# Kernel optimization log

Measured on AMD Instinct MI355X. Metric: run time of the kernel, lower is better.

Reference implementation:

```python
import jax, jax.numpy as jnp
import numpy as np

T = 1024      # tokens
H = 2048      # hidden_size
I = 1408      # moe_intermediate_size
E = 16        # n_routed_experts
K = 6         # num_experts_per_tok
SI = I * 2    # shared experts intermediate (n_shared_experts=2)


def setup_inputs() -> dict:
    key = jax.random.key(0)
    ks = jax.random.split(key, 8)
    s = 0.02
    return {
        "x": jax.random.normal(ks[0], (T, H), jnp.float32),
        "gate_w": jax.random.normal(ks[1], (E, H), jnp.float32) * s,
        "w_gate": jax.random.normal(ks[2], (E, I, H), jnp.float32) * s,
        "w_up": jax.random.normal(ks[3], (E, I, H), jnp.float32) * s,
        "w_down": jax.random.normal(ks[4], (E, H, I), jnp.float32) * s,
        "sw_gate": jax.random.normal(ks[5], (SI, H), jnp.float32) * s,
        "sw_up": jax.random.normal(ks[6], (SI, H), jnp.float32) * s,
        "sw_down": jax.random.normal(ks[7], (H, SI), jnp.float32) * s,
    }


def reference(x, gate_w, w_gate, w_up, w_down, sw_gate, sw_up, sw_down):
    t = x.shape[0]
    # ---- router: softmax over experts, top-k, renormalize (norm_topk_prob) ----
    logits = x @ gate_w.T                                   # [T, E]
    probs = jax.nn.softmax(logits.astype(jnp.float32), axis=-1)
    topw, topi = jax.lax.top_k(probs, K)                    # [T, K]
    topw = topw / jnp.sum(topw, axis=-1, keepdims=True)
    # per-token per-expert combine weight (0 for unselected experts)
    comb = jnp.zeros((t, E), probs.dtype).at[
        jnp.arange(t)[:, None], topi
    ].add(topw)                                             # [T, E]

    # ---- routed experts: SwiGLU MLP per expert, weighted combine ----
    g = jnp.einsum('th,eih->tei', x, w_gate)                # [T, E, I]
    u = jnp.einsum('th,eih->tei', x, w_up)                  # [T, E, I]
    h = jax.nn.silu(g) * u                                  # [T, E, I]
    routed = jnp.einsum('te,tei,ehi->th', comb, h, w_down)  # [T, H]

    # ---- shared experts (always-on SwiGLU MLP) ----
    shared = (jax.nn.silu(x @ sw_gate.T) * (x @ sw_up.T)) @ sw_down.T  # [T, H]

    return routed + shared
```

## Files before the change

### kernel.cpp

```cpp
#include <hip/hip_runtime.h>
#include <stdint.h>

#define T_TOK 1024
#define H_DIM 2048
#define I_DIM 1408
#define E_NUM 16
#define K_TOP 6
#define PADCAP 8192
#define NE_ALL 18

typedef __attribute__((ext_vector_type(8))) short short8;
typedef __attribute__((ext_vector_type(8))) unsigned short ushort8;
typedef __attribute__((ext_vector_type(4))) float f32x4;

__device__ __forceinline__ unsigned short f2b(float f) {
    unsigned u = __float_as_uint(f);
    u += 0x7fffu + ((u >> 16) & 1u);
    return (unsigned short)(u >> 16);
}
__device__ __forceinline__ float b2f(unsigned short s) {
    return __uint_as_float((unsigned)s << 16);
}

__device__ __forceinline__ unsigned cvt_pk2(float a, float b) {
    unsigned r;
    asm("v_cvt_pk_bf16_f32 %0, %1, %2" : "=v"(r) : "v"(a), "v"(b));
    return r;
}

typedef __attribute__((address_space(1))) const unsigned int as1_uint;
typedef __attribute__((address_space(3))) unsigned int as3_uint;
__device__ __forceinline__ void gload16(const void* g, void* l) {
    __builtin_amdgcn_global_load_lds((as1_uint*)g, (as3_uint*)l, 16, 0, 0);
}

__device__ __forceinline__ int xcd_swizzle(int bid, int nwg) {
    const int q = nwg >> 3, r = nwg & 7;
    const int xcd = bid & 7, k = bid >> 3;
    const int base = (xcd < r) ? xcd * (q + 1) : r * (q + 1) + (xcd - r) * q;
    return base + k;
}

__global__ __launch_bounds__(256) void router_kernel(
    const float* __restrict__ x, const float* __restrict__ gw,
    float* __restrict__ topw, int* __restrict__ eidx, int* __restrict__ slotarr,
    int* __restrict__ counts)
{
    const int t = blockIdx.x, tid = threadIdx.x;
    const int lane = tid & 63, wave = tid >> 6;
    float part[E_NUM];
#pragma unroll
    for (int e = 0; e < E_NUM; ++e) part[e] = 0.f;
    const float* xr = x + (size_t)t * H_DIM;
    for (int i = tid; i < H_DIM; i += 256) {
        float xv = xr[i];
#pragma unroll
        for (int e = 0; e < E_NUM; ++e) part[e] += xv * gw[e * H_DIM + i];
    }
    __shared__ float red[4][E_NUM];
#pragma unroll
    for (int e = 0; e < E_NUM; ++e) {
        float v = part[e];
        for (int off = 32; off; off >>= 1) v += __shfl_down(v, off);
        if (lane == 0) red[wave][e] = v;
    }
    __syncthreads();
    if (tid == 0) {
        float logits[E_NUM];
#pragma unroll
        for (int e = 0; e < E_NUM; ++e)
            logits[e] = red[0][e] + red[1][e] + red[2][e] + red[3][e];
        int sel[K_TOP]; float selv[K_TOP];
        unsigned used = 0;
        for (int k = 0; k < K_TOP; ++k) {
            int best = 0; float bv = -1e30f;
            for (int e = 0; e < E_NUM; ++e)
                if (!((used >> e) & 1u) && logits[e] > bv) { bv = logits[e]; best = e; }
            used |= 1u << best; sel[k] = best; selv[k] = bv;
        }
        float mx = selv[0], s = 0.f, w[K_TOP];
        for (int k = 0; k < K_TOP; ++k) { w[k] = expf(selv[k] - mx); s += w[k]; }
        float inv = 1.f / s;
        for (int k = 0; k < K_TOP; ++k) {
            int slot = atomicAdd(&counts[sel[k]], 1);
            topw[t * K_TOP + k] = w[k] * inv;
            eidx[t * K_TOP + k] = sel[k];
            slotarr[t * K_TOP + k] = slot;
        }
    }
}

__global__ void zero_counts_kernel(int* counts) {
    if (threadIdx.x < E_NUM) counts[threadIdx.x] = 0;
}

__global__ void prefix_kernel(const int* __restrict__ counts, int* __restrict__ offs) {
    if (threadIdx.x == 0) {
        int o = 0;
        for (int e = 0; e < E_NUM; ++e) { offs[e] = o; o += (counts[e] + 127) & ~127; }
        offs[E_NUM] = o;
    }
}

__global__ __launch_bounds__(256) void gather_cvt_kernel(
    const float* __restrict__ x, const int* __restrict__ eidx,
    const int* __restrict__ slotarr, const int* __restrict__ offs,
    ushort* __restrict__ Xall)
{
    const int b = blockIdx.x;
    int t; size_t row;
    if (b < T_TOK * K_TOP) {
        t = b / K_TOP;
        row = (size_t)offs[eidx[b]] + (size_t)slotarr[b];
    } else {
        t = b - T_TOK * K_TOP;
        row = (size_t)offs[E_NUM] + (size_t)t;
    }
    const float* src = x + (size_t)t * H_DIM;
    ushort* dst = Xall + row * H_DIM;
    const int i = threadIdx.x * 8;
    float4 f0 = *(const float4*)(src + i);
    float4 f1 = *(const float4*)(src + i + 4);
    ushort8 v;
    v[0] = f2b(f0.x); v[1] = f2b(f0.y); v[2] = f2b(f0.z); v[3] = f2b(f0.w);
    v[4] = f2b(f1.x); v[5] = f2b(f1.y); v[6] = f2b(f1.z); v[7] = f2b(f1.w);
    *(ushort8*)(dst + i) = v;
}

template<int DOWN>
__global__ __launch_bounds__(256, 2) void moe_gemm_kernel(
    const ushort* __restrict__ Abase,
    const float* __restrict__ Wr1, const float* __restrict__ Wr2,
    const float* __restrict__ Ws1, const float* __restrict__ Ws2,
    ushort* __restrict__ C1, ushort* __restrict__ C2,
    const int* __restrict__ counts, const int* __restrict__ offs,
    int nNT, int K, int ldc)
{
    __shared__ short Alds[2][128 * 64];
    __shared__ short Blds[2][128 * 64];

    const int work = xcd_swizzle(blockIdx.x, gridDim.x);
    const int slab = NE_ALL * 8;
    int nt = work / slab;
    const int rem = work - nt * slab;
    const int e = rem >> 3;
    const int mt = rem & 7;

    const int S = offs[E_NUM];
    const int M = (e < E_NUM) ? counts[e] : 1024;
    const int row0 = mt << 7;
    if (row0 >= M) return;
    const int crowbase = (e < E_NUM) ? offs[e] : S + ((e - E_NUM) << 10);
    const int arowbase = DOWN ? crowbase : ((e < E_NUM) ? offs[e] : S);

    const float* B; ushort* C; int ldb;
    if (DOWN) {
        ldb = (e < E_NUM) ? I_DIM : 2 * I_DIM;
        B = (e < E_NUM) ? Wr1 + (size_t)e * H_DIM * I_DIM
                        : Ws1 + (size_t)(e - E_NUM) * I_DIM;
        C = C1;
    } else {
        ldb = H_DIM;
        const float* Bg = (e < E_NUM) ? Wr1 + (size_t)e * I_DIM * H_DIM
                                      : Ws1 + (size_t)(e - E_NUM) * I_DIM * H_DIM;
        const float* Bu = (e < E_NUM) ? Wr2 + (size_t)e * I_DIM * H_DIM
                                      : Ws2 + (size_t)(e - E_NUM) * I_DIM * H_DIM;
        if (nt < nNT) { B = Bg; C = C1; }
        else          { B = Bu; C = C2; nt -= nNT; }
    }
    const int n0 = nt << 7;

    const int tid = threadIdx.x;
    const int lane = tid & 63;
    const int wave = tid >> 6;
    const int wm = wave & 1, wn = wave >> 1;
    const int l15 = lane & 15, lhi = lane >> 4;

    const char* __restrict__ Ab = (const char*)(Abase + (size_t)(arowbase + row0) * K);

    int aOff[4];
#pragma unroll
    for (int i = 0; i < 4; ++i) {
        const int chunk = wave * 4 + i;
        const int off = chunk * 1024 + lane * 16;
        const int r = off >> 7, s = (off >> 4) & 7;
        aOff[i] = r * K * 2 + ((s ^ (r & 7)) << 4);
    }

    const int r0 = (wave << 5) + (lane >> 3);
    const int sl = lane & 7;
    const float* Bg0 = B + (size_t)(n0 + r0) * ldb + (sl << 3);
    const int bLds0 = (r0 << 6) + ((sl ^ (r0 & 7)) << 3);

    f32x4 acc[4][4];
#pragma unroll
    for (int m = 0; m < 4; ++m)
#pragma unroll
        for (int n = 0; n < 4; ++n) acc[m][n] = (f32x4){0.f, 0.f, 0.f, 0.f};

    float4 breg[4][2];
    auto issueB = [&](int k0) {
#pragma unroll
        for (int j = 0; j < 4; ++j) {
            const float* src = Bg0 + (size_t)(j << 3) * ldb + k0;
            breg[j][0] = *(const float4*)src;
            breg[j][1] = *(const float4*)(src + 4);
        }
    };
    auto issueA = [&](int pb, int k0) {
#pragma unroll
        for (int i = 0; i < 4; ++i)
            gload16(Ab + (size_t)aOff[i] + (size_t)k0 * 2,
                    (char*)Alds[pb] + (wave * 4 + i) * 1024);
    };
    auto writeB = [&](int pb) {
        short* bl = Blds[pb];
#pragma unroll
        for (int j = 0; j < 4; ++j) {
            union { short8 s; unsigned u[4]; } w;
            w.u[0] = cvt_pk2(breg[j][0].x, breg[j][0].y);
            w.u[1] = cvt_pk2(breg[j][0].z, breg[j][0].w);
            w.u[2] = cvt_pk2(breg[j][1].x, breg[j][1].y);
            w.u[3] = cvt_pk2(breg[j][1].z, breg[j][1].w);
            *(short8*)&bl[bLds0 + (j << 9)] = w.s;
        }
    };

    const int nK = K >> 6;
    issueB(0);
    issueA(0, 0);
    writeB(0);
    __syncthreads();

    int p = 0;
    for (int kt = 0; kt < nK; ++kt) {
        const bool more = (kt + 1 < nK);
        if (more) {
            issueB((kt + 1) << 6);
            issueA(p ^ 1, (kt + 1) << 6);
        }
#pragma unroll
        for (int kk = 0; kk < 2; ++kk) {
            const int kb = (kk << 2) + lhi;
            short8 af[4], bfr[4];
#pragma unroll
            for (int m = 0; m < 4; ++m) {
                const int rA = (wm << 6) + (m << 4) + l15;
                af[m] = *(const short8*)&Alds[p][(rA << 6) + ((kb ^ (rA & 7)) << 3)];
            }
#pragma unroll
            for (int n = 0; n < 4; ++n) {
                const int rB = (wn << 6) + (n << 4) + l15;
                bfr[n] = *(const short8*)&Blds[p][(rB << 6) + ((kb ^ (rB & 7)) << 3)];
            }
#pragma unroll
            for (int m = 0; m < 4; ++m)
#pragma unroll
                for (int n = 0; n < 4; ++n)
                    acc[m][n] = __builtin_amdgcn_mfma_f32_16x16x32_bf16(
                        af[m], bfr[n], acc[m][n], 0, 0, 0);
        }
        if (more) writeB(p ^ 1);
        __syncthreads();
        p ^= 1;
    }

    const size_t cbase_col = (size_t)n0 + (wn << 6) + l15;
#pragma unroll
    for (int m = 0; m < 4; ++m) {
        const int rloc = (wm << 6) + (m << 4) + (lhi << 2);
#pragma unroll
        for (int j = 0; j < 4; ++j) {
            const int crow = row0 + rloc + j;
            if (crow >= M) continue;
            const size_t co = (size_t)(crowbase + crow) * ldc + cbase_col;
#pragma unroll
            for (int n = 0; n < 4; ++n) C[co + (n << 4)] = f2b(acc[m][n][j]);
        }
    }
}

__global__ __launch_bounds__(256) void silu_kernel(
    ushort* __restrict__ G, const ushort* __restrict__ U,
    const int* __restrict__ eidx, const int* __restrict__ slotarr,
    const int* __restrict__ offs)
{
    const int b = blockIdx.x;
    size_t row;
    if (b < T_TOK * K_TOP) {
        row = (size_t)offs[eidx[b]] + (size_t)slotarr[b];
    } else {
        row = (size_t)offs[E_NUM] + (size_t)(b - T_TOK * K_TOP);
    }
    ushort* g = G + row * I_DIM;
    const ushort* u = U + row * I_DIM;
    for (int i = threadIdx.x * 8; i < I_DIM; i += 2048) {
        ushort8 gv = *(const ushort8*)(g + i);
        ushort8 uv = *(const ushort8*)(u + i);
        ushort8 hv;
#pragma unroll
        for (int j = 0; j < 8; ++j) {
            float gf = b2f(gv[j]);
            float uf = b2f(uv[j]);
            float sf = gf / (1.f + expf(-gf));
            hv[j] = f2b(sf * uf);
        }
        *(ushort8*)(g + i) = hv;
    }
}

__global__ __launch_bounds__(256) void combine_kernel(
    float* __restrict__ out, const ushort* __restrict__ Y,
    const float* __restrict__ topw, const int* __restrict__ eidx,
    const int* __restrict__ slotarr, const int* __restrict__ offs)
{
    const int t = blockIdx.x;
    const int i = threadIdx.x * 8;
    const int S = offs[E_NUM];
    float acc[8];
    {
        ushort8 v0 = *(const ushort8*)(Y + ((size_t)S + t) * H_DIM + i);
        ushort8 v1 = *(const ushort8*)(Y + ((size_t)S + 1024 + t) * H_DIM + i);
#pragma unroll
        for (int j = 0; j < 8; ++j) acc[j] = b2f(v0[j]) + b2f(v1[j]);
    }
#pragma unroll
    for (int k = 0; k < K_TOP; ++k) {
        const float w = topw[t * K_TOP + k];
        const size_t row = (size_t)offs[eidx[t * K_TOP + k]] + (size_t)slotarr[t * K_TOP + k];
        ushort8 v = *(const ushort8*)(Y + row * H_DIM + i);
#pragma unroll
        for (int j = 0; j < 8; ++j) acc[j] += w * b2f(v[j]);
    }
    float* o = out + (size_t)t * H_DIM;
    float4 o0, o1;
    o0.x = acc[0]; o0.y = acc[1]; o0.z = acc[2]; o0.w = acc[3];
    o1.x = acc[4]; o1.y = acc[5]; o1.z = acc[6]; o1.w = acc[7];
    *(float4*)(o + i) = o0;
    *(float4*)(o + i + 4) = o1;
}

extern "C" void kernel_launch(void* const* d_in, const int* in_sizes, int n_in,
                              void* d_out, int out_size, void* d_ws, size_t ws_size,
                              hipStream_t stream) {
    const float* x       = (const float*)d_in[0];
    const float* gate_w  = (const float*)d_in[1];
    const float* w_gate  = (const float*)d_in[2];
    const float* w_up    = (const float*)d_in[3];
    const float* w_down  = (const float*)d_in[4];
    const float* sw_gate = (const float*)d_in[5];
    const float* sw_up   = (const float*)d_in[6];
    const float* sw_down = (const float*)d_in[7];
    float* out = (float*)d_out;

    char* p = (char*)d_ws;
    auto take = [&](size_t b) { char* r = p; p += (b + 255) & ~(size_t)255; return r; };
    int*    counts = (int*)take(32 * 4);
    int*    offs   = (int*)take(32 * 4);
    float*  topw   = (float*)take((size_t)T_TOK * K_TOP * 4);
    int*    eidx   = (int*)take((size_t)T_TOK * K_TOP * 4);
    int*    slot   = (int*)take((size_t)T_TOK * K_TOP * 4);
    ushort* Xall   = (ushort*)take((size_t)(PADCAP + 1024) * H_DIM * 2);
    ushort* G      = (ushort*)take((size_t)(PADCAP + 2048) * I_DIM * 2);
    ushort* U      = (ushort*)take((size_t)(PADCAP + 2048) * I_DIM * 2);
    ushort* Y      = (ushort*)take((size_t)(PADCAP + 2048) * H_DIM * 2);

    zero_counts_kernel<<<1, 64, 0, stream>>>(counts);
    router_kernel<<<T_TOK, 256, 0, stream>>>(x, gate_w, topw, eidx, slot, counts);
    prefix_kernel<<<1, 64, 0, stream>>>(counts, offs);
    gather_cvt_kernel<<<T_TOK * K_TOP + T_TOK, 256, 0, stream>>>(x, eidx, slot, offs, Xall);

    moe_gemm_kernel<0><<<22 * NE_ALL * 8, 256, 0, stream>>>(
        Xall, w_gate, w_up, sw_gate, sw_up, G, U, counts, offs, 11, H_DIM, I_DIM);
    silu_kernel<<<T_TOK * K_TOP + 2048, 256, 0, stream>>>(G, U, eidx, slot, offs);
    moe_gemm_kernel<1><<<16 * NE_ALL * 8, 256, 0, stream>>>(
        G, w_down, nullptr, sw_down, nullptr, Y, nullptr, counts, offs, 16, I_DIM, H_DIM);

    combine_kernel<<<T_TOK, 256, 0, stream>>>(out, Y, topw, eidx, slot, offs);
}
```

Baseline: 557.7 us.

## Enlarge MoE GEMM tiles to 256x128 with 512 threads and register-pipelined B

The MoE GEMM kernel now launches 512 threads per block and covers 256 token rows per tile instead of 128. This halves the number of M-tiles per expert, so each fp32 weight tile is fetched and converted to bf16 half as often. B now uses a single LDS buffer and is double-buffered in registers, while A stays double-buffered in LDS. Synchronisation uses explicit s_waitcnt and s_barrier, and the loop is unrolled by two. The trade-offs are more LDS and registers per block, which may lower occupancy, and more wasted rows on experts with few tokens.

```diff
diff --git a/kernel.cpp b/kernel.cpp
--- a/kernel.cpp
+++ b/kernel.cpp
@@ -33,6 +33,9 @@
 __device__ __forceinline__ void gload16(const void* g, void* l) {
     __builtin_amdgcn_global_load_lds((as1_uint*)g, (as3_uint*)l, 16, 0, 0);
 }
+
+#define WAIT_A_LGKM() asm volatile("s_waitcnt vmcnt(4) lgkmcnt(0)" ::: "memory")
+#define BAR() __builtin_amdgcn_s_barrier()
 
 __device__ __forceinline__ int xcd_swizzle(int bid, int nwg) {
     const int q = nwg >> 3, r = nwg & 7;
@@ -128,7 +131,7 @@
 }
 
 template<int DOWN>
-__global__ __launch_bounds__(256, 2) void moe_gemm_kernel(
+__global__ __launch_bounds__(512, 2) void moe_gemm_kernel(
     const ushort* __restrict__ Abase,
     const float* __restrict__ Wr1, const float* __restrict__ Wr2,
     const float* __restrict__ Ws1, const float* __restrict__ Ws2,
@@ -136,19 +139,19 @@
     const int* __restrict__ counts, const int* __restrict__ offs,
     int nNT, int K, int ldc)
 {
-    __shared__ short Alds[2][128 * 64];
-    __shared__ short Blds[2][128 * 64];
+    __shared__ short Alds[2][256 * 64];
+    __shared__ short Blds[128 * 64];
 
     const int work = xcd_swizzle(blockIdx.x, gridDim.x);
-    const int slab = NE_ALL * 8;
+    const int slab = NE_ALL * 4;
     int nt = work / slab;
     const int rem = work - nt * slab;
-    const int e = rem >> 3;
-    const int mt = rem & 7;
+    const int e = rem >> 2;
+    const int mt = rem & 3;
 
     const int S = offs[E_NUM];
     const int M = (e < E_NUM) ? counts[e] : 1024;
-    const int row0 = mt << 7;
+    const int row0 = mt << 8;
     if (row0 >= M) return;
     const int crowbase = (e < E_NUM) ? offs[e] : S + ((e - E_NUM) << 10);
     const int arowbase = DOWN ? crowbase : ((e < E_NUM) ? offs[e] : S);
@@ -173,7 +176,7 @@
     const int tid = threadIdx.x;
     const int lane = tid & 63;
     const int wave = tid >> 6;
-    const int wm = wave & 1, wn = wave >> 1;
+    const int wm = wave >> 1, wn = wave & 1;
     const int l15 = lane & 15, lhi = lane >> 4;
 
     const char* __restrict__ Ab = (const char*)(Abase + (size_t)(arowbase + row0) * K);
@@ -187,10 +190,15 @@
         aOff[i] = r * K * 2 + ((s ^ (r & 7)) << 4);
     }
 
-    const int r0 = (wave << 5) + (lane >> 3);
-    const int sl = lane & 7;
-    const float* Bg0 = B + (size_t)(n0 + r0) * ldb + (sl << 3);
-    const int bLds0 = (r0 << 6) + ((sl ^ (r0 & 7)) << 3);
+    const float* Bcell[2];
+    int bld[2];
+#pragma unroll
+    for (int c = 0; c < 2; ++c) {
+        const int cell = tid + (c << 9);
+        const int row = cell >> 3, sl = cell & 7;
+        Bcell[c] = B + (size_t)(n0 + row) * ldb + (sl << 3);
+        bld[c] = (row << 6) + ((sl ^ (row & 7)) << 3);
+    }
 
     f32x4 acc[4][4];
 #pragma unroll
@@ -198,47 +206,34 @@
 #pragma unroll
         for (int n = 0; n < 4; ++n) acc[m][n] = (f32x4){0.f, 0.f, 0.f, 0.f};
 
-    float4 breg[4][2];
-    auto issueB = [&](int k0) {
-#pragma unroll
-        for (int j = 0; j < 4; ++j) {
-            const float* src = Bg0 + (size_t)(j << 3) * ldb + k0;
-            breg[j][0] = *(const float4*)src;
-            breg[j][1] = *(const float4*)(src + 4);
-        }
-    };
-    auto issueA = [&](int pb, int k0) {
+    float4 brA[2][2], brB[2][2];
+
+    auto issueA = [&](int kt, int pb) {
 #pragma unroll
         for (int i = 0; i < 4; ++i)
-            gload16(Ab + (size_t)aOff[i] + (size_t)k0 * 2,
+            gload16(Ab + (size_t)aOff[i] + (size_t)(kt << 6) * 2,
                     (char*)Alds[pb] + (wave * 4 + i) * 1024);
     };
-    auto writeB = [&](int pb) {
-        short* bl = Blds[pb];
-#pragma unroll
-        for (int j = 0; j < 4; ++j) {
+    auto issueB = [&](int kt, float4 (&br)[2][2]) {
+#pragma unroll
+        for (int c = 0; c < 2; ++c) {
+            const float* src = Bcell[c] + (kt << 6);
+            br[c][0] = *(const float4*)src;
+            br[c][1] = *(const float4*)(src + 4);
+        }
+    };
+    auto writeB = [&](float4 (&br)[2][2]) {
+#pragma unroll
+        for (int c = 0; c < 2; ++c) {
             union { short8 s; unsigned u[4]; } w;
-            w.u[0] = cvt_pk2(breg[j][0].x, breg[j][0].y);
-            w.u[1] = cvt_pk2(breg[j][0].z, breg[j][0].w);
-            w.u[2] = cvt_pk2(breg[j][1].x, breg[j][1].y);
-            w.u[3] = cvt_pk2(breg[j][1].z, breg[j][1].w);
-            *(short8*)&bl[bLds0 + (j << 9)] = w.s;
+            w.u[0] = cvt_pk2(br[c][0].x, br[c][0].y);
+            w.u[1] = cvt_pk2(br[c][0].z, br[c][0].w);
+            w.u[2] = cvt_pk2(br[c][1].x, br[c][1].y);
+            w.u[3] = cvt_pk2(br[c][1].z, br[c][1].w);
+            *(short8*)&Blds[bld[c]] = w.s;
         }
     };
-
-    const int nK = K >> 6;
-    issueB(0);
-    issueA(0, 0);
-    writeB(0);
-    __syncthreads();
-
-    int p = 0;
-    for (int kt = 0; kt < nK; ++kt) {
-        const bool more = (kt + 1 < nK);
-        if (more) {
-            issueB((kt + 1) << 6);
-            issueA(p ^ 1, (kt + 1) << 6);
-        }
+    auto compute = [&](int p) {
 #pragma unroll
         for (int kk = 0; kk < 2; ++kk) {
             const int kb = (kk << 2) + lhi;
@@ -251,7 +246,7 @@
 #pragma unroll
             for (int n = 0; n < 4; ++n) {
                 const int rB = (wn << 6) + (n << 4) + l15;
-                bfr[n] = *(const short8*)&Blds[p][(rB << 6) + ((kb ^ (rB & 7)) << 3)];
+                bfr[n] = *(const short8*)&Blds[(rB << 6) + ((kb ^ (rB & 7)) << 3)];
             }
 #pragma unroll
             for (int m = 0; m < 4; ++m)
@@ -260,9 +255,32 @@
                     acc[m][n] = __builtin_amdgcn_mfma_f32_16x16x32_bf16(
                         af[m], bfr[n], acc[m][n], 0, 0, 0);
         }
-        if (more) writeB(p ^ 1);
-        __syncthreads();
-        p ^= 1;
+    };
+
+    const int nK = K >> 6;
+    issueB(0, brA);
+    issueA(0, 0);
+    writeB(brA);
+    issueB(nK > 1 ? 1 : 0, brB);
+    WAIT_A_LGKM();
+    BAR();
+
+    for (int tt = 0; tt < nK; tt += 2) {
+        issueA(min(tt + 1, nK - 1), 1);
+        issueB(min(tt + 2, nK - 1), brA);
+        compute(0);
+        BAR();
+        writeB(brB);
+        WAIT_A_LGKM();
+        BAR();
+
+        issueA(min(tt + 2, nK - 1), 0);
+        issueB(min(tt + 3, nK - 1), brB);
+        compute(1);
+        BAR();
+        writeB(brA);
+        WAIT_A_LGKM();
+        BAR();
     }
 
     const size_t cbase_col = (size_t)n0 + (wn << 6) + l15;
@@ -370,10 +388,10 @@
     prefix_kernel<<<1, 64, 0, stream>>>(counts, offs);
     gather_cvt_kernel<<<T_TOK * K_TOP + T_TOK, 256, 0, stream>>>(x, eidx, slot, offs, Xall);
 
-    moe_gemm_kernel<0><<<22 * NE_ALL * 8, 256, 0, stream>>>(
+    moe_gemm_kernel<0><<<22 * NE_ALL * 4, 512, 0, stream>>>(
         Xall, w_gate, w_up, sw_gate, sw_up, G, U, counts, offs, 11, H_DIM, I_DIM);
     silu_kernel<<<T_TOK * K_TOP + 2048, 256, 0, stream>>>(G, U, eidx, slot, offs);
-    moe_gemm_kernel<1><<<16 * NE_ALL * 8, 256, 0, stream>>>(
+    moe_gemm_kernel<1><<<16 * NE_ALL * 4, 512, 0, stream>>>(
         G, w_down, nullptr, sw_down, nullptr, Y, nullptr, counts, offs, 16, I_DIM, H_DIM);
 
     combine_kernel<<<T_TOK, 256, 0, stream>>>(out, Y, topw, eidx, slot, offs);
```

Result: slower. 648.1 us (+16.2%).

## Widen MoE GEMM tiles to 128x256 with 512 threads and padded intermediate stride

Applied to the files above, without the earlier changes.

The grouped GEMM goes from 256-thread 128x128 tiles to 512-thread 128x256 tiles. This halves the number of workgroups and means each A tile loaded into LDS is reused across twice as many output columns. The intermediate G/U buffers are padded to a 1536 column stride so the last N tile can write past 1408 without a bounds check, and B row indices are clamped for the edge tile. It also adds sched_barrier and setprio hints around the MFMA block. In exchange, LDS use per block doubles and the edge tiles do wasted work, which may lower occupancy.

```diff
diff --git a/kernel.cpp b/kernel.cpp
--- a/kernel.cpp
+++ b/kernel.cpp
@@ -4,6 +4,7 @@
 #define T_TOK 1024
 #define H_DIM 2048
 #define I_DIM 1408
+#define IPAD 1536
 #define E_NUM 16
 #define K_TOP 6
 #define PADCAP 8192
@@ -33,6 +34,8 @@
 __device__ __forceinline__ void gload16(const void* g, void* l) {
     __builtin_amdgcn_global_load_lds((as1_uint*)g, (as3_uint*)l, 16, 0, 0);
 }
+
+#define SCHED0() __builtin_amdgcn_sched_barrier(0)
 
 __device__ __forceinline__ int xcd_swizzle(int bid, int nwg) {
     const int q = nwg >> 3, r = nwg & 7;
@@ -128,16 +131,16 @@
 }
 
 template<int DOWN>
-__global__ __launch_bounds__(256, 2) void moe_gemm_kernel(
+__global__ __launch_bounds__(512, 2) void moe_gemm_kernel(
     const ushort* __restrict__ Abase,
     const float* __restrict__ Wr1, const float* __restrict__ Wr2,
     const float* __restrict__ Ws1, const float* __restrict__ Ws2,
     ushort* __restrict__ C1, ushort* __restrict__ C2,
     const int* __restrict__ counts, const int* __restrict__ offs,
-    int nNT, int K, int ldc)
+    int nNT, int lda, int K, int ldc)
 {
     __shared__ short Alds[2][128 * 64];
-    __shared__ short Blds[2][128 * 64];
+    __shared__ short Blds[2][256 * 64];
 
     const int work = xcd_swizzle(blockIdx.x, gridDim.x);
     const int slab = NE_ALL * 8;
@@ -153,44 +156,47 @@
     const int crowbase = (e < E_NUM) ? offs[e] : S + ((e - E_NUM) << 10);
     const int arowbase = DOWN ? crowbase : ((e < E_NUM) ? offs[e] : S);
 
-    const float* B; ushort* C; int ldb;
+    const float* B; ushort* C; int ldb, koff = 0, NB;
     if (DOWN) {
-        ldb = (e < E_NUM) ? I_DIM : 2 * I_DIM;
-        B = (e < E_NUM) ? Wr1 + (size_t)e * H_DIM * I_DIM
-                        : Ws1 + (size_t)(e - E_NUM) * I_DIM;
-        C = C1;
+        NB = H_DIM; C = C1;
+        if (e < E_NUM) { ldb = I_DIM; B = Wr1 + (size_t)e * H_DIM * I_DIM; }
+        else           { ldb = 2 * I_DIM; B = Ws1; koff = (e - E_NUM) * I_DIM; }
     } else {
-        ldb = H_DIM;
+        NB = I_DIM; ldb = H_DIM;
         const float* Bg = (e < E_NUM) ? Wr1 + (size_t)e * I_DIM * H_DIM
                                       : Ws1 + (size_t)(e - E_NUM) * I_DIM * H_DIM;
         const float* Bu = (e < E_NUM) ? Wr2 + (size_t)e * I_DIM * H_DIM
                                       : Ws2 + (size_t)(e - E_NUM) * I_DIM * H_DIM;
-        if (nt < nNT) { B = Bg; C = C1; }
-        else          { B = Bu; C = C2; nt -= nNT; }
-    }
-    const int n0 = nt << 7;
+        if (nt < nNT) { B = Bg; C = C1; } else { B = Bu; C = C2; nt -= nNT; }
+    }
+    const int n0 = nt << 8;
 
     const int tid = threadIdx.x;
     const int lane = tid & 63;
     const int wave = tid >> 6;
-    const int wm = wave & 1, wn = wave >> 1;
+    const int wm = wave >> 2, wn = wave & 3;
     const int l15 = lane & 15, lhi = lane >> 4;
 
-    const char* __restrict__ Ab = (const char*)(Abase + (size_t)(arowbase + row0) * K);
-
-    int aOff[4];
-#pragma unroll
-    for (int i = 0; i < 4; ++i) {
-        const int chunk = wave * 4 + i;
+    const char* __restrict__ Ab = (const char*)(Abase + (size_t)(arowbase + row0) * lda);
+
+    int aOff[2];
+#pragma unroll
+    for (int i = 0; i < 2; ++i) {
+        const int chunk = wave * 2 + i;
         const int off = chunk * 1024 + lane * 16;
         const int r = off >> 7, s = (off >> 4) & 7;
-        aOff[i] = r * K * 2 + ((s ^ (r & 7)) << 4);
-    }
-
-    const int r0 = (wave << 5) + (lane >> 3);
-    const int sl = lane & 7;
-    const float* Bg0 = B + (size_t)(n0 + r0) * ldb + (sl << 3);
-    const int bLds0 = (r0 << 6) + ((sl ^ (r0 & 7)) << 3);
+        aOff[i] = r * lda * 2 + ((s ^ (r & 7)) << 4);
+    }
+
+    const int brow = tid >> 3, bsl = tid & 7;
+    const float* Bc[4]; int bldw[4];
+#pragma unroll
+    for (int j = 0; j < 4; ++j) {
+        const int rl = brow + (j << 6);
+        const int rg = min(n0 + rl, NB - 1);
+        Bc[j] = B + (size_t)rg * ldb + koff + (bsl << 3);
+        bldw[j] = (rl << 6) + ((bsl ^ (rl & 7)) << 3);
+    }
 
     f32x4 acc[4][4];
 #pragma unroll
@@ -198,37 +204,62 @@
 #pragma unroll
         for (int n = 0; n < 4; ++n) acc[m][n] = (f32x4){0.f, 0.f, 0.f, 0.f};
 
-    float4 breg[4][2];
-    auto issueB = [&](int k0) {
+    float4 br[4][2];
+
+    auto issueA = [&](int kt, int pb) {
+#pragma unroll
+        for (int i = 0; i < 2; ++i)
+            gload16(Ab + (size_t)aOff[i] + (size_t)(kt << 7),
+                    (char*)Alds[pb] + (wave * 2 + i) * 1024);
+    };
+    auto issueB = [&](int kt) {
 #pragma unroll
         for (int j = 0; j < 4; ++j) {
-            const float* src = Bg0 + (size_t)(j << 3) * ldb + k0;
-            breg[j][0] = *(const float4*)src;
-            breg[j][1] = *(const float4*)(src + 4);
-        }
-    };
-    auto issueA = [&](int pb, int k0) {
-#pragma unroll
-        for (int i = 0; i < 4; ++i)
-            gload16(Ab + (size_t)aOff[i] + (size_t)k0 * 2,
-                    (char*)Alds[pb] + (wave * 4 + i) * 1024);
+            const float* src = Bc[j] + (kt << 6);
+            br[j][0] = *(const float4*)src;
+            br[j][1] = *(const float4*)(src + 4);
+        }
     };
     auto writeB = [&](int pb) {
-        short* bl = Blds[pb];
 #pragma unroll
         for (int j = 0; j < 4; ++j) {
             union { short8 s; unsigned u[4]; } w;
-            w.u[0] = cvt_pk2(breg[j][0].x, breg[j][0].y);
-            w.u[1] = cvt_pk2(breg[j][0].z, breg[j][0].w);
-            w.u[2] = cvt_pk2(breg[j][1].x, breg[j][1].y);
-            w.u[3] = cvt_pk2(breg[j][1].z, breg[j][1].w);
-            *(short8*)&bl[bLds0 + (j << 9)] = w.s;
+            w.u[0] = cvt_pk2(br[j][0].x, br[j][0].y);
+            w.u[1] = cvt_pk2(br[j][0].z, br[j][0].w);
+            w.u[2] = cvt_pk2(br[j][1].x, br[j][1].y);
+            w.u[3] = cvt_pk2(br[j][1].z, br[j][1].w);
+            *(short8*)&Blds[pb][bldw[j]] = w.s;
         }
     };
+    auto compute = [&](int p) {
+#pragma unroll
+        for (int kk = 0; kk < 2; ++kk) {
+            const int kb = (kk << 2) + lhi;
+            short8 af[4], bfr[4];
+#pragma unroll
+            for (int m = 0; m < 4; ++m) {
+                const int rA = (wm << 6) + (m << 4) + l15;
+                af[m] = *(const short8*)&Alds[p][(rA << 6) + ((kb ^ (rA & 7)) << 3)];
+            }
+#pragma unroll
+            for (int n = 0; n < 4; ++n) {
+                const int rB = (wn << 6) + (n << 4) + l15;
+                bfr[n] = *(const short8*)&Blds[p][(rB << 6) + ((kb ^ (rB & 7)) << 3)];
+            }
+            __builtin_amdgcn_s_setprio(1);
+#pragma unroll
+            for (int m = 0; m < 4; ++m)
+#pragma unroll
+                for (int n = 0; n < 4; ++n)
+                    acc[m][n] = __builtin_amdgcn_mfma_f32_16x16x32_bf16(
+                        af[m], bfr[n], acc[m][n], 0, 0, 0);
+            __builtin_amdgcn_s_setprio(0);
+        }
+    };
 
     const int nK = K >> 6;
-    issueB(0);
-    issueA(0, 0);
+    issueA(0, 0); SCHED0();
+    issueB(0); SCHED0();
     writeB(0);
     __syncthreads();
 
@@ -236,30 +267,10 @@
     for (int kt = 0; kt < nK; ++kt) {
         const bool more = (kt + 1 < nK);
         if (more) {
-            issueB((kt + 1) << 6);
-            issueA(p ^ 1, (kt + 1) << 6);
-        }
-#pragma unroll
-        for (int kk = 0; kk < 2; ++kk) {
-            const int kb = (kk << 2) + lhi;
-            short8 af[4], bfr[4];
-#pragma unroll
-            for (int m = 0; m < 4; ++m) {
-                const int rA = (wm << 6) + (m << 4) + l15;
-                af[m] = *(const short8*)&Alds[p][(rA << 6) + ((kb ^ (rA & 7)) << 3)];
-            }
-#pragma unroll
-            for (int n = 0; n < 4; ++n) {
-                const int rB = (wn << 6) + (n << 4) + l15;
-                bfr[n] = *(const short8*)&Blds[p][(rB << 6) + ((kb ^ (rB & 7)) << 3)];
-            }
-#pragma unroll
-            for (int m = 0; m < 4; ++m)
-#pragma unroll
-                for (int n = 0; n < 4; ++n)
-                    acc[m][n] = __builtin_amdgcn_mfma_f32_16x16x32_bf16(
-                        af[m], bfr[n], acc[m][n], 0, 0, 0);
-        }
+            issueA(kt + 1, p ^ 1); SCHED0();
+            issueB(kt + 1); SCHED0();
+        }
+        compute(p);
         if (more) writeB(p ^ 1);
         __syncthreads();
         p ^= 1;
@@ -292,9 +303,10 @@
     } else {
         row = (size_t)offs[E_NUM] + (size_t)(b - T_TOK * K_TOP);
     }
-    ushort* g = G + row * I_DIM;
-    const ushort* u = U + row * I_DIM;
-    for (int i = threadIdx.x * 8; i < I_DIM; i += 2048) {
+    ushort* g = G + row * IPAD;
+    const ushort* u = U + row * IPAD;
+    const int i = threadIdx.x * 8;
+    if (i < I_DIM) {
         ushort8 gv = *(const ushort8*)(g + i);
         ushort8 uv = *(const ushort8*)(u + i);
         ushort8 hv;
@@ -361,8 +373,8 @@
     int*    eidx   = (int*)take((size_t)T_TOK * K_TOP * 4);
     int*    slot   = (int*)take((size_t)T_TOK * K_TOP * 4);
     ushort* Xall   = (ushort*)take((size_t)(PADCAP + 1024) * H_DIM * 2);
-    ushort* G      = (ushort*)take((size_t)(PADCAP + 2048) * I_DIM * 2);
-    ushort* U      = (ushort*)take((size_t)(PADCAP + 2048) * I_DIM * 2);
+    ushort* G      = (ushort*)take((size_t)(PADCAP + 2048) * IPAD * 2);
+    ushort* U      = (ushort*)take((size_t)(PADCAP + 2048) * IPAD * 2);
     ushort* Y      = (ushort*)take((size_t)(PADCAP + 2048) * H_DIM * 2);
 
     zero_counts_kernel<<<1, 64, 0, stream>>>(counts);
@@ -370,11 +382,13 @@
     prefix_kernel<<<1, 64, 0, stream>>>(counts, offs);
     gather_cvt_kernel<<<T_TOK * K_TOP + T_TOK, 256, 0, stream>>>(x, eidx, slot, offs, Xall);
 
-    moe_gemm_kernel<0><<<22 * NE_ALL * 8, 256, 0, stream>>>(
-        Xall, w_gate, w_up, sw_gate, sw_up, G, U, counts, offs, 11, H_DIM, I_DIM);
+    moe_gemm_kernel<0><<<12 * NE_ALL * 8, 512, 0, stream>>>(
+        Xall, w_gate, w_up, sw_gate, sw_up, G, U, counts, offs,
+        6, H_DIM , H_DIM , IPAD );
     silu_kernel<<<T_TOK * K_TOP + 2048, 256, 0, stream>>>(G, U, eidx, slot, offs);
-    moe_gemm_kernel<1><<<16 * NE_ALL * 8, 256, 0, stream>>>(
-        G, w_down, nullptr, sw_down, nullptr, Y, nullptr, counts, offs, 16, I_DIM, H_DIM);
+    moe_gemm_kernel<1><<<8 * NE_ALL * 8, 512, 0, stream>>>(
+        G, w_down, nullptr, sw_down, nullptr, Y, nullptr, counts, offs,
+        8, IPAD , I_DIM , H_DIM );
 
     combine_kernel<<<T_TOK, 256, 0, stream>>>(out, Y, topw, eidx, slot, offs);
 }
```

Measured after the change: 564.0 us. About the same (+1.1%).
